# Optimization experiments

Measured on AMD Instinct MI355X. Metric: run time of the kernel, lower is better.

The kernel has to match this reference:

```python
import jax, jax.numpy as jnp
import numpy as np

D_MODEL = 1024
N_HEADS = 16
D_K = D_MODEL // N_HEADS  # 64
SCALE = 0.125             # attention_scale = 1/sqrt(d_k)
ROPE_BASE = 10000.0
NEG_INF = -1e30


def setup_inputs() -> dict:
    key = jax.random.key(0)
    k1, k2, k3 = jax.random.split(key, 3)
    B, S = 2, 2048
    x = jax.random.normal(k1, (B, S, D_MODEL), jnp.float32)
    # torch Linear(d_model, 3*d_model, bias=False): stored here as [in, out]
    w_qkv = jax.random.normal(k2, (D_MODEL, 3 * D_MODEL), jnp.float32) * (D_MODEL ** -0.5)
    w_o = jax.random.normal(k3, (D_MODEL, D_MODEL), jnp.float32) * (D_MODEL ** -0.5)
    return {"x": x, "w_qkv": w_qkv, "w_o": w_o}


def _rotary(x):
    # x: [B, H, S, D]; standard half-split rotary over sequence positions
    S, D = x.shape[2], x.shape[3]
    inv_freq = 1.0 / (ROPE_BASE ** (jnp.arange(0, D, 2, dtype=jnp.float32) / D))  # [D/2]
    freqs = jnp.arange(S, dtype=jnp.float32)[:, None] * inv_freq[None, :]          # [S, D/2]
    cos = jnp.cos(freqs)[None, None]  # [1,1,S,D/2]
    sin = jnp.sin(freqs)[None, None]
    x1, x2 = jnp.split(x, 2, axis=-1)
    return jnp.concatenate([x1 * cos + x2 * sin, -x1 * sin + x2 * cos], axis=-1).astype(x.dtype)


def reference(x, w_qkv, w_o):
    B, S, _ = x.shape
    qkv = x @ w_qkv                                        # [B,S,3*D_MODEL]
    qkv = qkv.reshape(B, S, 3, N_HEADS, D_K).transpose(2, 0, 3, 1, 4)  # [3,B,H,S,Dk]
    q, k, v = qkv[0], qkv[1], qkv[2]
    q = _rotary(q)
    k = _rotary(k)
    scores = jnp.einsum('bhqd,bhkd->bhqk', q, k) * SCALE   # [B,H,S,S]
    causal = jnp.tril(jnp.ones((S, S), dtype=bool))
    scores = jnp.where(causal, scores, NEG_INF)
    attn = jax.nn.softmax(scores, axis=-1)
    out = jnp.einsum('bhqk,bhkd->bhqd', attn, v)           # [B,H,S,Dk]
    out = out.transpose(0, 2, 1, 3).reshape(B, S, D_MODEL)
    return out @ w_o
```

## Files before the change

### kernel.cpp

```cpp
#include <hip/hip_runtime.h>

typedef short bf16x8 __attribute__((ext_vector_type(8)));
typedef short bf16x4 __attribute__((ext_vector_type(4)));
typedef float f32x4 __attribute__((ext_vector_type(4)));
typedef float f32x16 __attribute__((ext_vector_type(16)));
typedef int i32x4 __attribute__((ext_vector_type(4)));

#define DEVI static __device__ __forceinline__

DEVI unsigned short f2b(float f) {
  unsigned u = __float_as_uint(f);
  u += 0x7FFFu + ((u >> 16) & 1u);
  return (unsigned short)(u >> 16);
}

DEVI void gload16(const void* g, void* l) {
  __builtin_amdgcn_global_load_lds((const __attribute__((address_space(1))) void*)g,
                                   (__attribute__((address_space(3))) void*)l, 16, 0, 0);
}

DEVI void pl32swap(int a, int b, int& outa, int& outb) {
#if __has_builtin(__builtin_amdgcn_permlane32_swap)
  auto r = __builtin_amdgcn_permlane32_swap(a, b, false, false);
  outa = ((const int*)&r)[0];
  outb = ((const int*)&r)[1];
#else
  int bp = __shfl_xor(b, 32);
  int ap = __shfl_xor(a, 32);
  outa = (threadIdx.x & 32) ? bp : a;
  outb = (threadIdx.x & 32) ? b : ap;
#endif
}

DEVI float halfmax(float x) {
  int o0, o1;
  pl32swap(__float_as_int(x), __float_as_int(x), o0, o1);
  return fmaxf(__int_as_float(o0), __int_as_float(o1));
}
DEVI float halfsum(float x) {
  int o0, o1;
  pl32swap(__float_as_int(x), __float_as_int(x), o0, o1);
  return __int_as_float(o0) + __int_as_float(o1);
}

__global__ void rope_table_kernel(float* __restrict__ ct, float* __restrict__ st) {
  int i = blockIdx.x * 256 + threadIdx.x;
  int s = i >> 5, j = i & 31;
  float inv = powf(10000.0f, -(float)j * (1.0f / 32.0f));
  float a = (float)s * inv;
  ct[i] = cosf(a);
  st[i] = sinf(a);
}

__global__ void cvt_x_kernel(const float* __restrict__ x, unsigned short* __restrict__ xb) {
  int i = blockIdx.x * 256 + threadIdx.x;
  float4 v = ((const float4*)x)[i];
  ushort4 o;
  o.x = f2b(v.x); o.y = f2b(v.y); o.z = f2b(v.z); o.w = f2b(v.w);
  ((ushort4*)xb)[i] = o;
}

__global__ void transpose_kernel(const float* __restrict__ W, unsigned short* __restrict__ WT,
                                 int K, int N) {
  __shared__ float tile[32][33];
  int n0 = blockIdx.x * 32, k0 = blockIdx.y * 32;
  int tx = threadIdx.x, ty = threadIdx.y;
#pragma unroll
  for (int i = 0; i < 32; i += 8)
    tile[ty + i][tx] = W[(size_t)(k0 + ty + i) * N + n0 + tx];
  __syncthreads();
#pragma unroll
  for (int i = 0; i < 32; i += 8)
    WT[(size_t)(n0 + ty + i) * K + k0 + tx] = f2b(tile[tx][ty + i]);
}

__global__ __launch_bounds__(512, 2) void gemm_qkv_kernel(
    const unsigned short* __restrict__ Xb, const unsigned short* __restrict__ WT,
    const float* __restrict__ ct, const float* __restrict__ st,
    unsigned short* __restrict__ Qb, unsigned short* __restrict__ Kb,
    unsigned short* __restrict__ VTb) {
  __shared__ unsigned short As[2][256 * 64];
  __shared__ unsigned short Bs[2][256 * 64];
  const int tid = threadIdx.x;
  const int lane = tid & 63, wid = tid >> 6;
  const int flat = blockIdx.y * 12 + blockIdx.x;
  const int nf = (flat & 7) * 24 + (flat >> 3);
  const int bx = nf % 12, by = nf / 12;
  const int m0 = by * 256, n0 = bx * 256;
  const int wr = wid >> 2, wc = wid & 3;
  const int srow = lane >> 3;
  const int scc = ((lane & 7) ^ srow) * 8;
  const int rx = lane & 7;

  f32x4 acc[8][4] = {};

  auto stageA = [&](int k0, int nb, int i) {
    const int c = i * 8 + wid;
    const int row = c * 8 + srow;
    gload16(Xb + (size_t)(m0 + row) * 1024 + k0 + scc, (char*)As[nb] + c * 1024);
  };
  auto stageB = [&](int k0, int nb, int i) {
    const int c = i * 8 + wid;
    const int row = c * 8 + srow;
    gload16(WT + (size_t)(n0 + row) * 1024 + k0 + scc, (char*)Bs[nb] + c * 1024);
  };
  auto loadA = [&](const unsigned short* Ab, int q, bf16x8 af[2][2]) {
#pragma unroll
    for (int kk = 0; kk < 2; ++kk) {
      const int cc = ((kk * 4 + (lane >> 4)) ^ rx) * 8;
#pragma unroll
      for (int miL = 0; miL < 2; ++miL)
        af[miL][kk] = *(const bf16x8*)&Ab[(wr * 128 + (q * 2 + miL) * 16 + (lane & 15)) * 64 + cc];
    }
  };

#define QKV_MFMA_QUAD(Q)                                                      \
  __builtin_amdgcn_s_barrier();                                               \
  asm volatile("s_waitcnt lgkmcnt(0)" ::: "memory");                          \
  __builtin_amdgcn_s_setprio(1);                                              \
  _Pragma("unroll") for (int kk = 0; kk < 2; ++kk)                            \
    _Pragma("unroll") for (int miL = 0; miL < 2; ++miL)                       \
      _Pragma("unroll") for (int ni = 0; ni < 4; ++ni)                        \
        acc[(Q) * 2 + miL][ni] = __builtin_amdgcn_mfma_f32_16x16x32_bf16(     \
            af[miL][kk], bf[ni][kk], acc[(Q) * 2 + miL][ni], 0, 0, 0);        \
  __builtin_amdgcn_s_setprio(0);                                              \
  __builtin_amdgcn_s_barrier();

#pragma unroll
  for (int i = 0; i < 4; ++i) stageB(0, 0, i);
#pragma unroll
  for (int i = 0; i < 4; ++i) stageA(0, 0, i);
#pragma unroll
  for (int i = 0; i < 4; ++i) stageB(64, 1, i);
  stageA(64, 1, 0); stageA(64, 1, 2);
  asm volatile("s_waitcnt vmcnt(6)" ::: "memory");
  __builtin_amdgcn_s_barrier();

  for (int t = 0; t < 16; ++t) {
    const int b = t & 1;
    const unsigned short* Ab = As[b];
    const unsigned short* Bb = Bs[b];
    const int k1 = (t + 1) * 64, k2 = (t + 2) * 64;
    bf16x8 bf[4][2], af[2][2];

#pragma unroll
    for (int kk = 0; kk < 2; ++kk) {
      const int cc = ((kk * 4 + (lane >> 4)) ^ rx) * 8;
#pragma unroll
      for (int ni = 0; ni < 4; ++ni)
        bf[ni][kk] = *(const bf16x8*)&Bb[(wc * 64 + ni * 16 + (lane & 15)) * 64 + cc];
    }
    loadA(Ab, 0, af);
    if (t + 1 < 16) { stageA(k1, b ^ 1, 1); stageA(k1, b ^ 1, 3); }
    QKV_MFMA_QUAD(0)

    loadA(Ab, 1, af);
    if (t + 2 < 16) { stageB(k2, b, 0); stageB(k2, b, 1); }
    QKV_MFMA_QUAD(1)

    loadA(Ab, 2, af);
    if (t + 2 < 16) { stageB(k2, b, 2); stageB(k2, b, 3); }
    QKV_MFMA_QUAD(2)

    loadA(Ab, 3, af);
    if (t + 2 < 16) { stageA(k2, b, 0); stageA(k2, b, 2); }
    __builtin_amdgcn_s_barrier();
    asm volatile("s_waitcnt lgkmcnt(0)" ::: "memory");
    __builtin_amdgcn_s_setprio(1);
#pragma unroll
    for (int kk = 0; kk < 2; ++kk)
#pragma unroll
      for (int miL = 0; miL < 2; ++miL)
#pragma unroll
        for (int ni = 0; ni < 4; ++ni)
          acc[6 + miL][ni] = __builtin_amdgcn_mfma_f32_16x16x32_bf16(
              af[miL][kk], bf[ni][kk], acc[6 + miL][ni], 0, 0, 0);
    __builtin_amdgcn_s_setprio(0);
    if (t + 2 < 16) asm volatile("s_waitcnt vmcnt(6)" ::: "memory");
    else            asm volatile("s_waitcnt vmcnt(0)" ::: "memory");
    __builtin_amdgcn_s_barrier();
  }
#undef QKV_MFMA_QUAD

  const int n_base = n0 + wc * 64;
  const int ty = n_base >> 10;
  const int h = (n_base & 1023) >> 6;
  if (ty < 2) {
    unsigned short* dst = (ty == 0) ? Qb : Kb;
#pragma unroll
    for (int mi = 0; mi < 8; ++mi) {
      const int mrow = m0 + wr * 128 + mi * 16 + ((lane >> 4) << 2);
#pragma unroll
      for (int r = 0; r < 4; ++r) {
        const int m = mrow + r;
        const int s = m & 2047, bb = m >> 11;
        const size_t base = ((size_t)(bb * 16 + h) * 2048 + s) * 64;
#pragma unroll
        for (int ni = 0; ni < 2; ++ni) {
          const int j = ni * 16 + (lane & 15);
          const float c = ct[s * 32 + j], sn = st[s * 32 + j];
          const float x1 = acc[mi][ni][r], x2 = acc[mi][ni + 2][r];
          dst[base + j]      = f2b(x1 * c + x2 * sn);
          dst[base + j + 32] = f2b(-x1 * sn + x2 * c);
        }
      }
    }
  } else {
#pragma unroll
    for (int mi = 0; mi < 8; ++mi) {
      const int mrow = m0 + wr * 128 + mi * 16 + ((lane >> 4) << 2);
      const int s = mrow & 2047, bb = mrow >> 11;
#pragma unroll
      for (int ni = 0; ni < 4; ++ni) {
        const int d = ni * 16 + (lane & 15);
        ushort4 o;
        o.x = f2b(acc[mi][ni][0]); o.y = f2b(acc[mi][ni][1]);
        o.z = f2b(acc[mi][ni][2]); o.w = f2b(acc[mi][ni][3]);
        *(ushort4*)&VTb[((size_t)(bb * 16 + h) * 64 + d) * 2048 + s] = o;
      }
    }
  }
}

DEVI void gemm_mainloop(const unsigned short* __restrict__ A, const unsigned short* __restrict__ B,
                        unsigned short* As, unsigned short* Bs,
                        int m0, int n0, int lane, int wid, int wr, int wc,
                        f32x4 acc[4][4]) {
  const int srow = lane >> 3;
  const int scc = ((lane & 7) ^ srow) * 8;
  const int rx = lane & 7;
  auto stage = [&](int k0, int nb) {
    unsigned short* Ad = As + nb * 8192;
    unsigned short* Bd = Bs + nb * 8192;
#pragma unroll
    for (int i = 0; i < 4; ++i) {
      const int c = i * 4 + wid;
      const int row = c * 8 + srow;
      gload16(A + (size_t)(m0 + row) * 1024 + k0 + scc, (char*)Ad + c * 1024);
      gload16(B + (size_t)(n0 + row) * 1024 + k0 + scc, (char*)Bd + c * 1024);
    }
  };
  auto compute = [&](int nb) {
    const unsigned short* Ab = As + nb * 8192;
    const unsigned short* Bb = Bs + nb * 8192;
#pragma unroll
    for (int kk = 0; kk < 64; kk += 32) {
      const int cc = (((kk >> 3) + (lane >> 4)) ^ rx) * 8;
      bf16x8 a[4], b[4];
#pragma unroll
      for (int mi = 0; mi < 4; ++mi)
        a[mi] = *(const bf16x8*)&Ab[(wr * 64 + mi * 16 + (lane & 15)) * 64 + cc];
#pragma unroll
      for (int ni = 0; ni < 4; ++ni)
        b[ni] = *(const bf16x8*)&Bb[(wc * 64 + ni * 16 + (lane & 15)) * 64 + cc];
      __builtin_amdgcn_s_setprio(1);
#pragma unroll
      for (int mi = 0; mi < 4; ++mi)
#pragma unroll
        for (int ni = 0; ni < 4; ++ni)
          acc[mi][ni] = __builtin_amdgcn_mfma_f32_16x16x32_bf16(a[mi], b[ni], acc[mi][ni], 0, 0, 0);
      __builtin_amdgcn_s_setprio(0);
    }
  };
  stage(0, 0);
  stage(64, 1);
  for (int t = 0; t < 15; ++t) {
    asm volatile("s_waitcnt vmcnt(8)" ::: "memory");
    __builtin_amdgcn_s_barrier();
    compute(t & 1);
    __builtin_amdgcn_s_barrier();
    if (t < 14) stage((t + 2) * 64, t & 1);
  }
  asm volatile("s_waitcnt vmcnt(0)" ::: "memory");
  __builtin_amdgcn_s_barrier();
  compute(1);
}

DEVI void stage128(const unsigned short* __restrict__ Kh, const unsigned short* __restrict__ Vh,
                   int kbase, unsigned char* buf , int tid) {
  const int r = tid >> 3, c = tid & 7, cc = c ^ (r & 7);
  const int dst = (tid & ~63) * 16;
#pragma unroll
  for (int q = 0; q < 2; ++q) {
    unsigned char* b = buf + q * 16384;
    gload16(Kh + (size_t)(kbase + q * 64 + r) * 64 + cc * 8, b + dst);
    gload16(Vh + (size_t)r * 2048 + kbase + q * 64 + cc * 8, b + 8192 + dst);
  }
}

DEVI void attn_sub(const unsigned char* __restrict__ bufK, const unsigned char* __restrict__ bufV,
                   const bf16x8 qf[4], int s32, int kglob, bool diag, int qg, int ln, int hi,
                   float& m2, float& l_run, f32x16& acc0, f32x16& acc1) {
  const float C = 0.125f * 1.44269504f;
  const int rx = ln & 7;
  bf16x8 kf[4];
#pragma unroll
  for (int j = 0; j < 4; ++j) {
    const int cc = (2 * j + hi) ^ rx;
    kf[j] = *(const bf16x8*)(bufK + (s32 * 32 + ln) * 128 + cc * 16);
  }
  bf16x8 v0[2], v1[2];
#pragma unroll
  for (int p = 0; p < 2; ++p) {
    const int cc = (4 * s32 + 2 * p + hi) ^ rx;
    v0[p] = *(const bf16x8*)(bufV + ln * 128 + cc * 16);
    v1[p] = *(const bf16x8*)(bufV + (ln + 32) * 128 + cc * 16);
  }

  f32x16 stv = {};
  __builtin_amdgcn_s_setprio(1);
  stv = __builtin_amdgcn_mfma_f32_32x32x16_bf16(kf[0], qf[0], stv, 0, 0, 0);
  stv = __builtin_amdgcn_mfma_f32_32x32x16_bf16(kf[1], qf[1], stv, 0, 0, 0);
  stv = __builtin_amdgcn_mfma_f32_32x32x16_bf16(kf[2], qf[2], stv, 0, 0, 0);
  stv = __builtin_amdgcn_mfma_f32_32x32x16_bf16(kf[3], qf[3], stv, 0, 0, 0);
  __builtin_amdgcn_s_setprio(0);

  float sraw[16];
#pragma unroll
  for (int r = 0; r < 16; ++r) sraw[r] = stv[r];
  if (diag) {
#pragma unroll
    for (int r = 0; r < 16; ++r) {
      const int kg = kglob + (r & 3) + ((r >> 2) << 3) + (hi << 2);
      if (kg > qg) sraw[r] = -1e30f;
    }
  }
  float mraw = sraw[0];
#pragma unroll
  for (int r = 1; r < 16; ++r) mraw = fmaxf(mraw, sraw[r]);
  const float mloc = halfmax(mraw * C);
  if (__any(mloc > m2 + 11.5416f)) {
    const float mnew = fmaxf(m2, mloc);
    const float sc = exp2f(m2 - mnew);
    l_run *= sc;
#pragma unroll
    for (int r = 0; r < 16; ++r) { acc0[r] *= sc; acc1[r] *= sc; }
    m2 = mnew;
  }
  float p[16], ps = 0.f;
#pragma unroll
  for (int r = 0; r < 16; ++r) { p[r] = exp2f(fmaf(sraw[r], C, -m2)); ps += p[r]; }
  l_run += halfsum(ps);

  int cw[8];
#pragma unroll
  for (int i = 0; i < 8; ++i)
    asm("v_cvt_pk_bf16_f32 %0, %1, %2" : "=v"(cw[i]) : "v"(p[2 * i]), "v"(p[2 * i + 1]));
  int a0, a1, b0, b1, a2, a3, b2, b3;
  pl32swap(cw[0], cw[2], a0, b0);
  pl32swap(cw[1], cw[3], a1, b1);
  pl32swap(cw[4], cw[6], a2, b2);
  pl32swap(cw[5], cw[7], a3, b3);
  const bf16x8 pa0 = __builtin_bit_cast(bf16x8, (i32x4){a0, a1, b0, b1});
  const bf16x8 pa1 = __builtin_bit_cast(bf16x8, (i32x4){a2, a3, b2, b3});

  __builtin_amdgcn_s_setprio(1);
  acc0 = __builtin_amdgcn_mfma_f32_32x32x16_bf16(v0[0], pa0, acc0, 0, 0, 0);
  acc0 = __builtin_amdgcn_mfma_f32_32x32x16_bf16(v0[1], pa1, acc0, 0, 0, 0);
  acc1 = __builtin_amdgcn_mfma_f32_32x32x16_bf16(v1[0], pa0, acc1, 0, 0, 0);
  acc1 = __builtin_amdgcn_mfma_f32_32x32x16_bf16(v1[1], pa1, acc1, 0, 0, 0);
  __builtin_amdgcn_s_setprio(0);
}

DEVI void write_partial(float* M, int slot, const f32x16& a0, const f32x16& a1,
                        float m2, float l) {
#pragma unroll
  for (int r = 0; r < 16; ++r) { M[slot + r] = a0[r]; M[slot + 16 + r] = a1[r]; }
  M[slot + 32] = m2;
  M[slot + 33] = l;
}

DEVI void write_merged(unsigned short* __restrict__ Ob, const float* M, int slot,
                       const f32x16& acc0, const f32x16& acc1, float m2, float l_run,
                       int bh, int q0, int ln, int hi) {
  const float mp = M[slot + 32], lp = M[slot + 33];
  const float m = fmaxf(m2, mp);
  const float eo = exp2f(m2 - m), ep = exp2f(mp - m);
  const float il = 1.0f / (l_run * eo + lp * ep);
  const int b = bh >> 4, h = bh & 15;
  unsigned short* ob = Ob + ((size_t)(b * 2048 + q0 + ln)) * 1024 + h * 64;
#pragma unroll
  for (int g = 0; g < 4; ++g) {
    ushort4 o0, o1;
    o0.x = f2b((acc0[4 * g + 0] * eo + M[slot + 4 * g + 0] * ep) * il);
    o0.y = f2b((acc0[4 * g + 1] * eo + M[slot + 4 * g + 1] * ep) * il);
    o0.z = f2b((acc0[4 * g + 2] * eo + M[slot + 4 * g + 2] * ep) * il);
    o0.w = f2b((acc0[4 * g + 3] * eo + M[slot + 4 * g + 3] * ep) * il);
    o1.x = f2b((acc1[4 * g + 0] * eo + M[slot + 16 + 4 * g + 0] * ep) * il);
    o1.y = f2b((acc1[4 * g + 1] * eo + M[slot + 16 + 4 * g + 1] * ep) * il);
    o1.z = f2b((acc1[4 * g + 2] * eo + M[slot + 16 + 4 * g + 2] * ep) * il);
    o1.w = f2b((acc1[4 * g + 3] * eo + M[slot + 16 + 4 * g + 3] * ep) * il);
    *(ushort4*)&ob[8 * g + 4 * hi]      = o0;
    *(ushort4*)&ob[32 + 8 * g + 4 * hi] = o1;
  }
}

__global__ __launch_bounds__(512) void attn_kernel(
    const unsigned short* __restrict__ Qb, const unsigned short* __restrict__ Kb,
    const unsigned short* __restrict__ VTb, unsigned short* __restrict__ Ob) {
  __shared__ unsigned char smem[2][2][16384];
  const int tid = threadIdx.x;
  const int lane = tid & 63, wid = tid >> 6;
  const int ln = lane & 31, hi = lane >> 5;
  const int s = wid & 3, half = wid >> 2;
  const int bh = blockIdx.x;
  const int p = blockIdx.y;
  const int jA = 15 - p, jB = p;
  const unsigned short* Qh = Qb + (size_t)bh * 2048 * 64;
  const unsigned short* Kh = Kb + (size_t)bh * 2048 * 64;
  const unsigned short* Vh = VTb + (size_t)bh * 64 * 2048;

  f32x16 aA0 = {}, aA1 = {}, aB0 = {}, aB1 = {};
  float mA = -1e30f, lA = 0.f, mB = -1e30f, lB = 0.f;
  int it = 0;

  auto load_q = [&](int q0, bf16x8 qf[4]) {
    const unsigned short* pq = Qh + (size_t)(q0 + ln) * 64 + hi * 8;
#pragma unroll
    for (int t = 0; t < 4; ++t) qf[t] = *(const bf16x8*)(pq + t * 16);
  };
  auto run_phase = [&](int j, const bf16x8 qf[4], f32x16& acc0, f32x16& acc1,
                       float& m2, float& l_run, int q0, int nextFirst) {
    const int qg = q0 + ln;
    const int top = q0 >> 5;
    for (int kb = 0; kb <= j; ++kb, ++it) {
      const int nxt = (kb < j) ? (kb + 1) * 128 : nextFirst;
      if (nxt >= 0) stage128(Kh, Vh, nxt, &smem[(it + 1) & 1][0][0], tid);
      const unsigned char* bufK = &smem[it & 1][half][0];
      const unsigned char* bufV = bufK + 8192;
      const int t64 = 2 * kb + half;
#pragma unroll
      for (int s32 = 0; s32 < 2; ++s32) {
        const int g32 = 2 * t64 + s32;
        if (g32 <= top)
          attn_sub(bufK, bufV, qf, s32, g32 * 32, g32 == top, qg, ln, hi, m2, l_run, acc0, acc1);
      }
      __syncthreads();
    }
  };

  bf16x8 qfA[4];
  load_q(jA * 128 + s * 32, qfA);
  stage128(Kh, Vh, 0, &smem[0][0][0], tid);
  __syncthreads();
  run_phase(jA, qfA, aA0, aA1, mA, lA, jA * 128 + s * 32, 0);
  bf16x8 qfB[4];
  load_q(jB * 128 + s * 32, qfB);
  run_phase(jB, qfB, aB0, aB1, mB, lB, jB * 128 + s * 32, -1);

  float* M = (float*)&smem[0][0][0];
  const int slot = (s * 64 + lane) * 34;
  if (half == 1) write_partial(M, slot, aA0, aA1, mA, lA);
  __syncthreads();
  if (half == 0) write_merged(Ob, M, slot, aA0, aA1, mA, lA, bh, jA * 128 + s * 32, ln, hi);
  __syncthreads();
  if (half == 0) write_partial(M, slot, aB0, aB1, mB, lB);
  __syncthreads();
  if (half == 1) write_merged(Ob, M, slot, aB0, aB1, mB, lB, bh, jB * 128 + s * 32, ln, hi);
}

__global__ __launch_bounds__(256) void gemm_out_kernel(
    const unsigned short* __restrict__ Ob, const unsigned short* __restrict__ WoT,
    float* __restrict__ out) {
  __shared__ unsigned short As[2][128 * 64];
  __shared__ unsigned short Bs[2][128 * 64];
  const int lane = threadIdx.x & 63, wid = threadIdx.x >> 6;
  const int m0 = blockIdx.y * 128, n0 = blockIdx.x * 128;
  const int wr = wid >> 1, wc = wid & 1;
  f32x4 acc[4][4] = {};
  gemm_mainloop(Ob, WoT, &As[0][0], &Bs[0][0], m0, n0, lane, wid, wr, wc, acc);
#pragma unroll
  for (int mi = 0; mi < 4; ++mi) {
    const int mrow = m0 + wr * 64 + mi * 16 + ((lane >> 4) << 2);
#pragma unroll
    for (int ni = 0; ni < 4; ++ni) {
      const int n = n0 + wc * 64 + ni * 16 + (lane & 15);
#pragma unroll
      for (int r = 0; r < 4; ++r)
        out[(size_t)(mrow + r) * 1024 + n] = acc[mi][ni][r];
    }
  }
}

extern "C" void kernel_launch(void* const* d_in, const int* in_sizes, int n_in,
                              void* d_out, int out_size, void* d_ws, size_t ws_size,
                              hipStream_t stream) {
  const float* x     = (const float*)d_in[0];
  const float* w_qkv = (const float*)d_in[1];
  const float* w_o   = (const float*)d_in[2];
  float* out = (float*)d_out;
  char* ws = (char*)d_ws;

  const size_t MB = 1 << 20;
  float* ct = (float*)(ws);
  float* st = (float*)(ws + (256 << 10));
  unsigned short* Xb  = (unsigned short*)(ws + (512 << 10));
  unsigned short* WqT = (unsigned short*)(ws + (512 << 10) + 8  * MB);
  unsigned short* WoT = (unsigned short*)(ws + (512 << 10) + 14 * MB);
  unsigned short* Qb  = (unsigned short*)(ws + (512 << 10) + 16 * MB);
  unsigned short* Kb  = (unsigned short*)(ws + (512 << 10) + 24 * MB);
  unsigned short* VTb = (unsigned short*)(ws + (512 << 10) + 32 * MB);
  unsigned short* Ob  = Xb;

  rope_table_kernel<<<dim3(256), dim3(256), 0, stream>>>(ct, st);
  cvt_x_kernel<<<dim3(4096), dim3(256), 0, stream>>>(x, Xb);
  transpose_kernel<<<dim3(96, 32), dim3(32, 8), 0, stream>>>(w_qkv, WqT, 1024, 3072);
  transpose_kernel<<<dim3(32, 32), dim3(32, 8), 0, stream>>>(w_o, WoT, 1024, 1024);
  gemm_qkv_kernel<<<dim3(12, 16), dim3(512), 0, stream>>>(Xb, WqT, ct, st, Qb, Kb, VTb);
  attn_kernel<<<dim3(32, 8), dim3(512), 0, stream>>>(Qb, Kb, VTb, Ob);
  gemm_out_kernel<<<dim3(8, 32), dim3(256), 0, stream>>>(Ob, WoT, out);
}
```

Baseline: 124.3 us.

## Stage QKV epilogue through LDS for coalesced stores, interleave rope table, defer row-sum reduction

The QKV GEMM epilogue now writes rotary-applied Q/K and transposed V tiles into padded LDS slabs, reusing the A/B staging buffers. It then emits 16-byte coalesced global stores instead of scattered 2-byte and 8-byte writes. The cos/sin tables are interleaved into a single float2 array so each lookup is one load. In attention, the cross-half row-sum reduction is moved out of the inner loop and done once at the end, and the max reduction only runs when a rescale is triggered. This adds LDS traffic and reuses shared memory after the main loop, which needs correct barriers.

```diff
diff --git a/kernel.cpp b/kernel.cpp
--- a/kernel.cpp
+++ b/kernel.cpp
@@ -43,13 +43,12 @@
   return __int_as_float(o0) + __int_as_float(o1);
 }
 
-__global__ void rope_table_kernel(float* __restrict__ ct, float* __restrict__ st) {
+__global__ void rope_table_kernel(float2* __restrict__ cst) {
   int i = blockIdx.x * 256 + threadIdx.x;
   int s = i >> 5, j = i & 31;
   float inv = powf(10000.0f, -(float)j * (1.0f / 32.0f));
   float a = (float)s * inv;
-  ct[i] = cosf(a);
-  st[i] = sinf(a);
+  cst[i] = make_float2(cosf(a), sinf(a));
 }
 
 __global__ void cvt_x_kernel(const float* __restrict__ x, unsigned short* __restrict__ xb) {
@@ -76,7 +75,7 @@
 
 __global__ __launch_bounds__(512, 2) void gemm_qkv_kernel(
     const unsigned short* __restrict__ Xb, const unsigned short* __restrict__ WT,
-    const float* __restrict__ ct, const float* __restrict__ st,
+    const float2* __restrict__ cst,
     unsigned short* __restrict__ Qb, unsigned short* __restrict__ Kb,
     unsigned short* __restrict__ VTb) {
   __shared__ unsigned short As[2][256 * 64];
@@ -182,41 +181,68 @@
   }
 #undef QKV_MFMA_QUAD
 
+  unsigned short* slab = (wid < 4) ? (&As[0][0] + wid * 8192)
+                                   : (&Bs[0][0] + (wid - 4) * 8192);
   const int n_base = n0 + wc * 64;
   const int ty = n_base >> 10;
   const int h = (n_base & 1023) >> 6;
+  const int qrow = (lane >> 4) << 2;
+  const int l15 = lane & 15;
+  const int rlane = lane >> 3, clane = lane & 7;
+
   if (ty < 2) {
     unsigned short* dst = (ty == 0) ? Qb : Kb;
 #pragma unroll
-    for (int mi = 0; mi < 8; ++mi) {
-      const int mrow = m0 + wr * 128 + mi * 16 + ((lane >> 4) << 2);
-#pragma unroll
-      for (int r = 0; r < 4; ++r) {
-        const int m = mrow + r;
-        const int s = m & 2047, bb = m >> 11;
-        const size_t base = ((size_t)(bb * 16 + h) * 2048 + s) * 64;
-#pragma unroll
-        for (int ni = 0; ni < 2; ++ni) {
-          const int j = ni * 16 + (lane & 15);
-          const float c = ct[s * 32 + j], sn = st[s * 32 + j];
-          const float x1 = acc[mi][ni][r], x2 = acc[mi][ni + 2][r];
-          dst[base + j]      = f2b(x1 * c + x2 * sn);
-          dst[base + j + 32] = f2b(-x1 * sn + x2 * c);
+    for (int g = 0; g < 2; ++g) {
+      const int rowg = m0 + wr * 128 + g * 64;
+      const int s_half = rowg & 2047, bb = rowg >> 11;
+#pragma unroll
+      for (int miL = 0; miL < 4; ++miL) {
+        const int mi = g * 4 + miL;
+        const int rl0 = miL * 16 + qrow;
+#pragma unroll
+        for (int r = 0; r < 4; ++r) {
+#pragma unroll
+          for (int ni = 0; ni < 2; ++ni) {
+            const int j = ni * 16 + l15;
+            const float2 cs = cst[(s_half + rl0 + r) * 32 + j];
+            const float x1 = acc[mi][ni][r], x2 = acc[mi][ni + 2][r];
+            slab[(rl0 + r) * 72 + j]      = f2b(x1 * cs.x + x2 * cs.y);
+            slab[(rl0 + r) * 72 + j + 32] = f2b(-x1 * cs.y + x2 * cs.x);
+          }
         }
       }
+      unsigned short* dp = dst + ((size_t)(bb * 16 + h) * 2048 + s_half) * 64;
+#pragma unroll
+      for (int i = 0; i < 8; ++i) {
+        const int row = i * 8 + rlane;
+        const bf16x8 v = *(const bf16x8*)&slab[row * 72 + clane * 8];
+        *(bf16x8*)&dp[row * 64 + clane * 8] = v;
+      }
     }
   } else {
 #pragma unroll
-    for (int mi = 0; mi < 8; ++mi) {
-      const int mrow = m0 + wr * 128 + mi * 16 + ((lane >> 4) << 2);
-      const int s = mrow & 2047, bb = mrow >> 11;
-#pragma unroll
-      for (int ni = 0; ni < 4; ++ni) {
-        const int d = ni * 16 + (lane & 15);
-        ushort4 o;
-        o.x = f2b(acc[mi][ni][0]); o.y = f2b(acc[mi][ni][1]);
-        o.z = f2b(acc[mi][ni][2]); o.w = f2b(acc[mi][ni][3]);
-        *(ushort4*)&VTb[((size_t)(bb * 16 + h) * 64 + d) * 2048 + s] = o;
+    for (int g = 0; g < 2; ++g) {
+      const int rowg = m0 + wr * 128 + g * 64;
+      const int s_half = rowg & 2047, bb = rowg >> 11;
+#pragma unroll
+      for (int miL = 0; miL < 4; ++miL) {
+        const int mi = g * 4 + miL;
+        const int rl0 = miL * 16 + qrow;
+#pragma unroll
+        for (int ni = 0; ni < 4; ++ni) {
+          const int d = ni * 16 + l15;
+#pragma unroll
+          for (int r = 0; r < 4; ++r)
+            slab[d * 72 + rl0 + r] = f2b(acc[mi][ni][r]);
+        }
+      }
+      unsigned short* vp = VTb + (size_t)(bb * 16 + h) * 64 * 2048 + s_half;
+#pragma unroll
+      for (int i = 0; i < 8; ++i) {
+        const int d = i * 8 + rlane;
+        const bf16x8 v = *(const bf16x8*)&slab[d * 72 + clane * 8];
+        *(bf16x8*)&vp[(size_t)d * 2048 + clane * 8] = v;
       }
     }
   }
@@ -277,7 +303,7 @@
 }
 
 DEVI void stage128(const unsigned short* __restrict__ Kh, const unsigned short* __restrict__ Vh,
-                   int kbase, unsigned char* buf , int tid) {
+                   int kbase, unsigned char* buf, int tid) {
   const int r = tid >> 3, c = tid & 7, cc = c ^ (r & 7);
   const int dst = (tid & ~63) * 16;
 #pragma unroll
@@ -328,9 +354,9 @@
   float mraw = sraw[0];
 #pragma unroll
   for (int r = 1; r < 16; ++r) mraw = fmaxf(mraw, sraw[r]);
-  const float mloc = halfmax(mraw * C);
-  if (__any(mloc > m2 + 11.5416f)) {
-    const float mnew = fmaxf(m2, mloc);
+  const float mlc = mraw * C;
+  if (__any(mlc > m2 + 11.5416f)) {
+    const float mnew = fmaxf(m2, halfmax(mlc));
     const float sc = exp2f(m2 - mnew);
     l_run *= sc;
 #pragma unroll
@@ -340,7 +366,7 @@
   float p[16], ps = 0.f;
 #pragma unroll
   for (int r = 0; r < 16; ++r) { p[r] = exp2f(fmaf(sraw[r], C, -m2)); ps += p[r]; }
-  l_run += halfsum(ps);
+  l_run += ps;
 
   int cw[8];
 #pragma unroll
@@ -448,6 +474,9 @@
   load_q(jB * 128 + s * 32, qfB);
   run_phase(jB, qfB, aB0, aB1, mB, lB, jB * 128 + s * 32, -1);
 
+  lA = halfsum(lA);
+  lB = halfsum(lB);
+
   float* M = (float*)&smem[0][0][0];
   const int slot = (s * 64 + lane) * 34;
   if (half == 1) write_partial(M, slot, aA0, aA1, mA, lA);
@@ -492,8 +521,7 @@
   char* ws = (char*)d_ws;
 
   const size_t MB = 1 << 20;
-  float* ct = (float*)(ws);
-  float* st = (float*)(ws + (256 << 10));
+  float2* cst = (float2*)(ws);
   unsigned short* Xb  = (unsigned short*)(ws + (512 << 10));
   unsigned short* WqT = (unsigned short*)(ws + (512 << 10) + 8  * MB);
   unsigned short* WoT = (unsigned short*)(ws + (512 << 10) + 14 * MB);
@@ -502,11 +530,11 @@
   unsigned short* VTb = (unsigned short*)(ws + (512 << 10) + 32 * MB);
   unsigned short* Ob  = Xb;
 
-  rope_table_kernel<<<dim3(256), dim3(256), 0, stream>>>(ct, st);
+  rope_table_kernel<<<dim3(256), dim3(256), 0, stream>>>(cst);
   cvt_x_kernel<<<dim3(4096), dim3(256), 0, stream>>>(x, Xb);
   transpose_kernel<<<dim3(96, 32), dim3(32, 8), 0, stream>>>(w_qkv, WqT, 1024, 3072);
   transpose_kernel<<<dim3(32, 32), dim3(32, 8), 0, stream>>>(w_o, WoT, 1024, 1024);
-  gemm_qkv_kernel<<<dim3(12, 16), dim3(512), 0, stream>>>(Xb, WqT, ct, st, Qb, Kb, VTb);
+  gemm_qkv_kernel<<<dim3(12, 16), dim3(512), 0, stream>>>(Xb, WqT, cst, Qb, Kb, VTb);
   attn_kernel<<<dim3(32, 8), dim3(512), 0, stream>>>(Qb, Kb, VTb, Ob);
   gemm_out_kernel<<<dim3(8, 32), dim3(256), 0, stream>>>(Ob, WoT, out);
 }
```

Result: faster. 120.5 us (-3.1%).
